# Optimization experiments

Hardware: AMD Instinct MI355X
Metric: run time of the kernel (lower is better)

Reference implementation:

```python
import jax, jax.numpy as jnp
import numpy as np

B, C, D_IN, T = 8, 4, 256, 1024
D_MODEL = 256


def setup_inputs() -> dict:
    key = jax.random.key(0)
    k_x, k_m, k_wq, k_bq, k_wo, k_bo = jax.random.split(key, 6)
    x = jax.random.normal(k_x, (B, C, D_IN, T), dtype=jnp.float32)
    mask = jax.random.randint(k_m, (B, C, T, T), 0, 2) == 1  # bool, True = masked
    s_in = 1.0 / np.sqrt(D_IN)
    s_md = 1.0 / np.sqrt(D_MODEL)
    w_qkv = jax.random.uniform(k_wq, (3 * D_MODEL, D_IN), jnp.float32, -s_in, s_in)
    b_qkv = jax.random.uniform(k_bq, (3 * D_MODEL,), jnp.float32, -s_in, s_in)
    w_out = jax.random.uniform(k_wo, (D_MODEL, D_MODEL), jnp.float32, -s_md, s_md)
    b_out = jax.random.uniform(k_bo, (D_MODEL,), jnp.float32, -s_md, s_md)
    return {"x": x, "mask": mask, "w_qkv": w_qkv, "b_qkv": b_qkv,
            "w_out": w_out, "b_out": b_out}


def reference(x, mask, w_qkv, b_qkv, w_out, b_out):
    # x: (B, C, d_in, t) -> (B, C, t, d_in)
    xt = jnp.swapaxes(x, -1, -2)
    qkv = jnp.einsum('bctd,ed->bcte', xt, w_qkv) + b_qkv  # (B,C,t,3*d_model)
    q, k, v = jnp.split(qkv, 3, axis=-1)
    scale = 1.0 / jnp.sqrt(jnp.asarray(q.shape[-1], dtype=q.dtype))
    scores = jnp.einsum('bcqd,bckd->bcqk', q, k) * scale  # (B,C,t,t)
    scores = jnp.where(mask, -jnp.inf, scores)
    attn = jax.nn.softmax(scores, axis=-1)
    out = jnp.einsum('bcqk,bckd->bcqd', attn, v)          # (B,C,t,d_model)
    return jnp.einsum('bcqd,ed->bcqe', out, w_out) + b_out
```

## Files before the change

kernel.cpp:

```cpp
#include <hip/hip_runtime.h>
#include <hip/hip_bf16.h>

#define TT 1024
#define DM 256
#define BCN 32

typedef __attribute__((ext_vector_type(8))) short short8;
typedef __attribute__((ext_vector_type(4))) short short4v;
typedef __attribute__((ext_vector_type(4))) float f32x4;

__device__ __forceinline__ void wg_barrier_lds() {
  asm volatile("s_waitcnt lgkmcnt(0)\n\ts_barrier" ::: "memory");
}

__device__ __forceinline__ short bf16b(float f) {
  __hip_bfloat16 h = __float2bfloat16(f);
  return *(short*)&h;
}

__device__ __forceinline__ void dma16(void* l, const void* g) {
  __builtin_amdgcn_global_load_lds(
      (const __attribute__((address_space(1))) void*)g,
      (__attribute__((address_space(3))) void*)l, 16, 0, 0);
}
__device__ __forceinline__ void dma4(void* l, const void* g) {
  __builtin_amdgcn_global_load_lds(
      (const __attribute__((address_space(1))) void*)g,
      (__attribute__((address_space(3))) void*)l, 4, 0, 0);
}

__global__ __launch_bounds__(256, 8) void maskprep_kernel(
    const int* __restrict__ mask, unsigned* __restrict__ mbits,
    const float* __restrict__ w_qkv, const float* __restrict__ w_out,
    __hip_bfloat16* __restrict__ Wb, __hip_bfloat16* __restrict__ Wo)
{
  const int tid = threadIdx.x;

  if (blockIdx.x >= 512) {
    int idx = (blockIdx.x - 512) * 256 + tid;
    const float* src;
    __hip_bfloat16* dst;
    if (idx < 24576) { src = w_qkv; dst = Wb; }
    else { idx -= 24576; src = w_out; dst = Wo; }
    const int r = idx >> 5, ch = idx & 31;
    const float4* wv4 = (const float4*)src + (size_t)r * 64 + ch * 2;
    const float4 f0 = wv4[0], f1 = wv4[1];
    short8 pk;
    pk[0] = bf16b(f0.x); pk[1] = bf16b(f0.y);
    pk[2] = bf16b(f0.z); pk[3] = bf16b(f0.w);
    pk[4] = bf16b(f1.x); pk[5] = bf16b(f1.y);
    pk[6] = bf16b(f1.z); pk[7] = bf16b(f1.w);
    *(short8*)&dst[(size_t)r * 256 + ((ch ^ (r & 7)) << 3)] = pk;
    return;
  }

  __shared__ unsigned Wlds[64][33];
  const int m = blockIdx.x;
  const int bc = m >> 4, q0 = (m & 15) * 64;
  const int w = tid >> 6, l = tid & 63;
  const int4* base =
      (const int4*)(mask + (size_t)(bc * 1024 + q0 + w * 16) * 1024) + l;
  int4 v[4], n[4];
#pragma unroll
  for (int s = 0; s < 4; ++s) v[s] = base[s * 64];
#pragma unroll 1
  for (int rr = 0; rr < 16; ++rr) {
    if (rr < 15) {
      const int4* nb = base + (rr + 1) * 256;
#pragma unroll
      for (int s = 0; s < 4; ++s) n[s] = nb[s * 64];
    }
    const int ql = w * 16 + rr;
#pragma unroll
    for (int s = 0; s < 4; ++s) {
      const unsigned long long bx = __ballot(v[s].x != 0);
      const unsigned long long by = __ballot(v[s].y != 0);
      const unsigned long long bz = __ballot(v[s].z != 0);
      const unsigned long long bw = __ballot(v[s].w != 0);
      if (l < 8) {
        const unsigned word =
            (unsigned)((bx >> (8 * l)) & 0xFF) |
            ((unsigned)((by >> (8 * l)) & 0xFF) << 8) |
            ((unsigned)((bz >> (8 * l)) & 0xFF) << 16) |
            ((unsigned)((bw >> (8 * l)) & 0xFF) << 24);
        Wlds[ql][s * 8 + l] = word;
      }
    }
#pragma unroll
    for (int s = 0; s < 4; ++s) v[s] = n[s];
  }
  __syncthreads();
  unsigned* mb = mbits + (size_t)bc * 32 * 1024 + q0;
#pragma unroll
  for (int i = 0; i < 8; ++i) {
    const int idx = tid + i * 256, j = idx >> 6, ql = idx & 63;
    mb[(size_t)j * 1024 + ql] = Wlds[ql][j];
  }
}

__global__ __launch_bounds__(256, 2) void qkv_kernel(
    const float* __restrict__ x, const __hip_bfloat16* __restrict__ Wb,
    const float* __restrict__ b_qkv,
    __hip_bfloat16* __restrict__ Qb, __hip_bfloat16* __restrict__ Kb,
    __hip_bfloat16* __restrict__ Vtb)
{
  const int tid = threadIdx.x;
  __shared__ __attribute__((aligned(16))) __hip_bfloat16 Xs[64][264];
  __shared__ __attribute__((aligned(16))) __hip_bfloat16 Wd[2][32 * 256];
  __shared__ __attribute__((aligned(16))) float bls[768];

  const int tt = blockIdx.x & 15, bc = blockIdx.x >> 4;
  const int t0 = tt * 64;
  const int w = tid >> 6, l = tid & 63, quad = l >> 4, lm = l & 15;
  const int lm7 = lm & 7;

  const char* Wg = (const char*)Wb;
  auto wissue = [&](int it, int buf) {
    const char* g = Wg + (size_t)it * 16384 + w * 4096 + l * 16;
    char* d = (char*)&Wd[buf][0] + w * 4096;
#pragma unroll
    for (int i = 0; i < 4; ++i) dma16(d + i * 1024, g + i * 1024);
  };

  wissue(0, 0);
  wissue(1, 1);

  if (tid < 192) {
    const float4 bv = *(const float4*)(b_qkv + tid * 4);
    *(float4*)&bls[tid * 4] = bv;
  }

  {
    const float* xbc = x + (size_t)bc * DM * TT;
    const int t4 = (tid & 15) * 4;
    for (int s = 0; s < 4; ++s) {
      const int d4 = (tid >> 4) * 4 + s * 64;
      f32x4 f[4];
#pragma unroll
      for (int r = 0; r < 4; ++r)
        f[r] = *(const f32x4*)(xbc + (size_t)(d4 + r) * TT + t0 + t4);
#pragma unroll
      for (int r = 0; r < 4; ++r) {
        short4v pk;
#pragma unroll
        for (int c = 0; c < 4; ++c) pk[c] = bf16b(f[c][r]);
        *(short4v*)&Xs[t4 + r][d4] = pk;
      }
    }
  }

#pragma unroll 1
  for (int it = 0; it < 24; ++it) {
    const int buf = it & 1;
    if (it == 0)
      asm volatile("s_waitcnt vmcnt(4)" ::: "memory");
    else if (it < 23)
      asm volatile("s_waitcnt vmcnt(6)" ::: "memory");
    else
      asm volatile("s_waitcnt vmcnt(2)" ::: "memory");
    wg_barrier_lds();

    const int e0 = it * 32;
    const bool vmode = (it >= 16);
    const __hip_bfloat16* WT = &Wd[buf][0];
    f32x4 acc[2] = {};
#pragma unroll
    for (int ks = 0; ks < 8; ++ks) {
      const int k = ks * 32 + quad * 8;
      const short8 xa = *(const short8*)&Xs[w * 16 + lm][k];
      const int c = ((ks * 4 + quad) ^ lm7) << 3;
#pragma unroll
      for (int nt = 0; nt < 2; ++nt) {
        const short8 wb2 = *(const short8*)&WT[(nt * 16 + lm) * 256 + c];
        acc[nt] = vmode
            ? __builtin_amdgcn_mfma_f32_16x16x32_bf16(xa, wb2, acc[nt], 0, 0, 0)
            : __builtin_amdgcn_mfma_f32_16x16x32_bf16(wb2, xa, acc[nt], 0, 0, 0);
      }
    }

    if (it < 8) {
      const int t = t0 + w * 16 + lm;
#pragma unroll
      for (int nt = 0; nt < 2; ++nt) {
        const int ebase = e0 + nt * 16 + quad * 4;
        const f32x4 bb = *(const f32x4*)&bls[ebase];
        short4v pk;
#pragma unroll
        for (int r = 0; r < 4; ++r) pk[r] = bf16b(acc[nt][r] + bb[r]);
        *(short4v*)&Qb[((size_t)bc * TT + t) * DM + ebase] = pk;
      }
    } else if (!vmode) {
      const int t = t0 + w * 16 + lm;
#pragma unroll
      for (int nt = 0; nt < 2; ++nt) {
        const int eg = e0 + nt * 16 + quad * 4;
        const int eK = eg - 256;
        const f32x4 bb = *(const f32x4*)&bls[eg];
        short4v pk;
#pragma unroll
        for (int r = 0; r < 4; ++r) pk[r] = bf16b(acc[nt][r] + bb[r]);
        const int ch = eK >> 3;
        const int off = (((ch ^ (t & 7)) << 3) | (eK & 7));
        *(short4v*)&Kb[((size_t)bc * TT + t) * DM + off] = pk;
      }
    } else {
      const int tb = w * 16 + quad * 4;
      const int kb = tt * 2 + (tb >> 5), tloc = tb & 31;
#pragma unroll
      for (int nt = 0; nt < 2; ++nt) {
        const int e = (e0 - 512) + nt * 16 + lm;
        const float bq = bls[512 + e];
        short4v pk;
#pragma unroll
        for (int r = 0; r < 4; ++r) pk[r] = bf16b(acc[nt][r] + bq);
        *(short4v*)&Vtb[(((size_t)bc * 32 + kb) * 256 + e) * 32 + tloc] = pk;
      }
    }

    wg_barrier_lds();
    if (it < 22) wissue(it + 2, buf);
  }
}

__global__ __launch_bounds__(256, 2) void attn_kernel(
    const __hip_bfloat16* __restrict__ Qb, const __hip_bfloat16* __restrict__ Kb,
    const __hip_bfloat16* __restrict__ Vtb, const unsigned* __restrict__ Mbits,
    const __hip_bfloat16* __restrict__ Wob, const float* __restrict__ b_out,
    float* __restrict__ out)
{
  const int fid = blockIdx.x;
  const int xcd = fid & 7, slot = fid >> 3;
  const int bc = xcd * 4 + (slot >> 4);
  const int qt = slot & 15;
  const int q0 = qt * 64;

  __shared__ __attribute__((aligned(16))) char smem[72192];
  __hip_bfloat16* Ks = (__hip_bfloat16*)smem;
  __hip_bfloat16* Vs = (__hip_bfloat16*)(smem + 32768);
  __hip_bfloat16 (*Ps)[40] = (__hip_bfloat16(*)[40])(smem + 65536);
  unsigned* Msb = (unsigned*)(smem + 70656);
  float* bout = (float*)(smem + 71168);
  __hip_bfloat16 (*Os)[264] = (__hip_bfloat16(*)[264])smem;
  __hip_bfloat16* Wo = (__hip_bfloat16*)(smem + 33792);

  const int tid = threadIdx.x, w = tid >> 6, l = tid & 63;
  const int quad = l >> 4, lm = l & 15, lm7 = lm & 7;
  const int trow = w * 16 + lm;

  if (tid < 64) {
    const f32x4 bv = *(const f32x4*)(b_out + tid * 4);
    *(f32x4*)&bout[tid * 4] = bv;
  }

  const __hip_bfloat16* Qg =
      Qb + ((size_t)bc * TT + q0 + trow) * DM + quad * 8;
  short8 qf[8];
#pragma unroll
  for (int ks = 0; ks < 8; ++ks) qf[ks] = *(const short8*)(Qg + ks * 32);

  const char* KgT = (const char*)(Kb + (size_t)bc * TT * DM);
  const char* VgT = (const char*)(Vtb + (size_t)bc * TT * DM);
  const unsigned* MgT = Mbits + ((size_t)bc * 32) * 1024 + q0;

  short8 ones;
#pragma unroll
  for (int i = 0; i < 8; ++i) ones[i] = (short)0x3F80;

  f32x4 Oa[16] = {};
  f32x4 Ol = {};

  auto issue = [&](int j, int buf) {
    const char* kg = KgT + (size_t)j * 16384 + w * 4096 + l * 16;
    const char* vg = VgT + (size_t)j * 16384 + w * 4096 + l * 16;
    char* kl = (char*)Ks + buf * 16384 + w * 4096;
    char* vl = (char*)Vs + buf * 16384 + w * 4096;
#pragma unroll
    for (int i = 0; i < 4; ++i) dma16(kl + i * 1024, kg + i * 1024);
#pragma unroll
    for (int i = 0; i < 4; ++i) dma16(vl + i * 1024, vg + i * 1024);
    dma4((char*)Msb + buf * 256, MgT + (size_t)j * 1024 + l);
  };

  auto compute = [&](int buf) {
    const __hip_bfloat16* KT = Ks + buf * 8192;
    const __hip_bfloat16* VT = Vs + buf * 8192;
    f32x4 Sa0 = {}, Sa1 = {};
#pragma unroll
    for (int ks = 0; ks < 8; ++ks) {
      const int c = ((ks * 4 + quad) ^ lm7) << 3;
      const short8 a0 = *(const short8*)&KT[lm * 256 + c];
      const short8 a1 = *(const short8*)&KT[(lm + 16) * 256 + c];
      Sa0 = __builtin_amdgcn_mfma_f32_16x16x32_bf16(a0, qf[ks], Sa0, 0, 0, 0);
      Sa1 = __builtin_amdgcn_mfma_f32_16x16x32_bf16(a1, qf[ks], Sa1, 0, 0, 0);
    }
    const unsigned mw = Msb[buf * 64 + trow];
#pragma unroll
    for (int nt = 0; nt < 2; ++nt) {
      const f32x4 Sa = nt ? Sa1 : Sa0;
      short4v pk;
#pragma unroll
      for (int r = 0; r < 4; ++r) {
        const float p = ((mw >> (nt * 4 + quad + 8 * r)) & 1u)
                            ? 0.f
                            : __expf(fmaf(Sa[r], 0.0625f, -8.0f));
        pk[r] = bf16b(p);
      }
      *(short4v*)&Ps[trow][nt * 16 + quad * 4] = pk;
    }
    const short8 pf = *(const short8*)&Ps[trow][quad * 8];
#pragma unroll
    for (int ct = 0; ct < 16; ++ct) {
      const short8 a = *(const short8*)&VT[(ct * 16 + lm) * 32 + quad * 8];
      Oa[ct] = __builtin_amdgcn_mfma_f32_16x16x32_bf16(a, pf, Oa[ct], 0, 0, 0);
    }
    Ol = __builtin_amdgcn_mfma_f32_16x16x32_bf16(ones, pf, Ol, 0, 0, 0);
  };

  issue(0, 0);
  issue(1, 1);
#pragma unroll 1
  for (int j = 0; j < 32; ++j) {
    const int buf = j & 1;
    if (j < 31)
      asm volatile("s_waitcnt vmcnt(9)" ::: "memory");
    else
      asm volatile("s_waitcnt vmcnt(0)" ::: "memory");
    asm volatile("s_barrier" ::: "memory");
    compute(buf);
    wg_barrier_lds();
    if (j < 30) issue(j + 2, buf);
  }

  const char* WoG = (const char*)Wob;
  auto pissue = [&](int it, int buf) {
    const char* g = WoG + (size_t)it * 16384 + w * 4096 + l * 16;
    char* d = (char*)Wo + buf * 16384 + w * 4096;
#pragma unroll
    for (int i = 0; i < 4; ++i) dma16(d + i * 1024, g + i * 1024);
  };
  pissue(0, 0);
  pissue(1, 1);

  const float inv = 1.0f / Ol[0];
#pragma unroll
  for (int ct = 0; ct < 16; ++ct) {
    short4v pk;
#pragma unroll
    for (int r = 0; r < 4; ++r) pk[r] = bf16b(Oa[ct][r] * inv);
    *(short4v*)&Os[trow][ct * 16 + quad * 4] = pk;
  }
  wg_barrier_lds();

  short8 osr[8];
#pragma unroll
  for (int ks = 0; ks < 8; ++ks)
    osr[ks] = *(const short8*)&Os[trow][ks * 32 + quad * 8];

  float* outp = out + ((size_t)bc * TT + q0 + trow) * DM;
#pragma unroll 1
  for (int it = 0; it < 8; ++it) {
    const int buf = it & 1;
    if (it == 0)
      asm volatile("s_waitcnt vmcnt(4)" ::: "memory");
    else if (it < 7)
      asm volatile("s_waitcnt vmcnt(6)" ::: "memory");
    else
      asm volatile("s_waitcnt vmcnt(2)" ::: "memory");
    wg_barrier_lds();

    f32x4 acc[2] = {};
#pragma unroll
    for (int ks = 0; ks < 8; ++ks) {
      const int c = ((ks * 4 + quad) ^ lm7) << 3;
#pragma unroll
      for (int nt = 0; nt < 2; ++nt) {
        const short8 wa = *(const short8*)&Wo[buf * 8192 + (nt * 16 + lm) * 256 + c];
        acc[nt] = __builtin_amdgcn_mfma_f32_16x16x32_bf16(wa, osr[ks], acc[nt], 0, 0, 0);
      }
    }
#pragma unroll
    for (int nt = 0; nt < 2; ++nt) {
      const int fb = it * 32 + nt * 16 + quad * 4;
      const f32x4 bb = *(const f32x4*)&bout[fb];
      float4 o;
      o.x = acc[nt][0] + bb[0];
      o.y = acc[nt][1] + bb[1];
      o.z = acc[nt][2] + bb[2];
      o.w = acc[nt][3] + bb[3];
      *(float4*)&outp[fb] = o;
    }

    wg_barrier_lds();
    if (it < 6) pissue(it + 2, buf);
  }
}

extern "C" void kernel_launch(void* const* d_in, const int* in_sizes, int n_in,
                              void* d_out, int out_size, void* d_ws, size_t ws_size,
                              hipStream_t stream) {
  const float* x = (const float*)d_in[0];
  const int* mask = (const int*)d_in[1];
  const float* w_qkv = (const float*)d_in[2];
  const float* b_qkv = (const float*)d_in[3];
  const float* w_out = (const float*)d_in[4];
  const float* b_out = (const float*)d_in[5];
  float* out = (float*)d_out;

  const size_t N = (size_t)BCN * TT * DM;
  __hip_bfloat16* Qb  = (__hip_bfloat16*)d_ws;
  __hip_bfloat16* Kb  = Qb + N;
  __hip_bfloat16* Vtb = Kb + N;
  unsigned* Mbits     = (unsigned*)(Vtb + N);
  __hip_bfloat16* Wbp = (__hip_bfloat16*)(Mbits + (size_t)BCN * 32 * 1024);
  __hip_bfloat16* Wob = Wbp + 768 * 256;

  maskprep_kernel<<<dim3(640), dim3(256), 0, stream>>>(mask, Mbits,
                                                       w_qkv, w_out, Wbp, Wob);
  qkv_kernel<<<dim3(512), dim3(256), 0, stream>>>(x, Wbp, b_qkv, Qb, Kb, Vtb);
  attn_kernel<<<dim3(512), dim3(256), 0, stream>>>(Qb, Kb, Vtb, Mbits,
                                                   Wob, b_out, out);
}
```

Measured before the change: 322.4 us.

## Process 128 query rows per attention block to reuse K/V tiles

Each attention workgroup now handles two 64-row query halves, sharing each loaded K/V tile and mask chunk between them and halving the grid to 256 blocks. This is meant to halve global/LDS traffic for K and V per query row. It doubles accumulator and Q-fragment registers, risking spills or lower occupancy, and leaves only one block per CU. The output projection is run twice sequentially, once per half.

```diff
diff --git a/kernel.cpp b/kernel.cpp
--- a/kernel.cpp
+++ b/kernel.cpp
@@ -230,16 +230,16 @@
 {
   const int fid = blockIdx.x;
   const int xcd = fid & 7, slot = fid >> 3;
-  const int bc = xcd * 4 + (slot >> 4);
-  const int qt = slot & 15;
-  const int q0 = qt * 64;
-
-  __shared__ __attribute__((aligned(16))) char smem[72192];
+  const int bc = xcd * 4 + (slot >> 3);
+  const int qt = slot & 7;
+  const int q0 = qt * 128;
+
+  __shared__ __attribute__((aligned(16))) char smem[77824];
   __hip_bfloat16* Ks = (__hip_bfloat16*)smem;
   __hip_bfloat16* Vs = (__hip_bfloat16*)(smem + 32768);
   __hip_bfloat16 (*Ps)[40] = (__hip_bfloat16(*)[40])(smem + 65536);
-  unsigned* Msb = (unsigned*)(smem + 70656);
-  float* bout = (float*)(smem + 71168);
+  unsigned* Msb = (unsigned*)(smem + 75776);
+  float* bout = (float*)(smem + 76800);
   __hip_bfloat16 (*Os)[264] = (__hip_bfloat16(*)[264])smem;
   __hip_bfloat16* Wo = (__hip_bfloat16*)(smem + 33792);
 
@@ -252,11 +252,14 @@
     *(f32x4*)&bout[tid * 4] = bv;
   }
 
-  const __hip_bfloat16* Qg =
-      Qb + ((size_t)bc * TT + q0 + trow) * DM + quad * 8;
-  short8 qf[8];
-#pragma unroll
-  for (int ks = 0; ks < 8; ++ks) qf[ks] = *(const short8*)(Qg + ks * 32);
+  short8 qf[2][8];
+#pragma unroll
+  for (int h = 0; h < 2; ++h) {
+    const __hip_bfloat16* Qg =
+        Qb + ((size_t)bc * TT + q0 + h * 64 + trow) * DM + quad * 8;
+#pragma unroll
+    for (int ks = 0; ks < 8; ++ks) qf[h][ks] = *(const short8*)(Qg + ks * 32);
+  }
 
   const char* KgT = (const char*)(Kb + (size_t)bc * TT * DM);
   const char* VgT = (const char*)(Vtb + (size_t)bc * TT * DM);
@@ -266,8 +269,8 @@
 #pragma unroll
   for (int i = 0; i < 8; ++i) ones[i] = (short)0x3F80;
 
-  f32x4 Oa[16] = {};
-  f32x4 Ol = {};
+  f32x4 Oa[32] = {};
+  f32x4 Ol[2] = {};
 
   auto issue = [&](int j, int buf) {
     const char* kg = KgT + (size_t)j * 16384 + w * 4096 + l * 16;
@@ -278,42 +281,51 @@
     for (int i = 0; i < 4; ++i) dma16(kl + i * 1024, kg + i * 1024);
 #pragma unroll
     for (int i = 0; i < 4; ++i) dma16(vl + i * 1024, vg + i * 1024);
-    dma4((char*)Msb + buf * 256, MgT + (size_t)j * 1024 + l);
+    dma4((char*)Msb + buf * 512, MgT + (size_t)j * 1024 + l);
+    dma4((char*)Msb + buf * 512 + 256, MgT + (size_t)j * 1024 + 64 + l);
   };
 
   auto compute = [&](int buf) {
     const __hip_bfloat16* KT = Ks + buf * 8192;
     const __hip_bfloat16* VT = Vs + buf * 8192;
-    f32x4 Sa0 = {}, Sa1 = {};
+    f32x4 Sa[2][2] = {};
 #pragma unroll
     for (int ks = 0; ks < 8; ++ks) {
       const int c = ((ks * 4 + quad) ^ lm7) << 3;
       const short8 a0 = *(const short8*)&KT[lm * 256 + c];
       const short8 a1 = *(const short8*)&KT[(lm + 16) * 256 + c];
-      Sa0 = __builtin_amdgcn_mfma_f32_16x16x32_bf16(a0, qf[ks], Sa0, 0, 0, 0);
-      Sa1 = __builtin_amdgcn_mfma_f32_16x16x32_bf16(a1, qf[ks], Sa1, 0, 0, 0);
-    }
-    const unsigned mw = Msb[buf * 64 + trow];
-#pragma unroll
-    for (int nt = 0; nt < 2; ++nt) {
-      const f32x4 Sa = nt ? Sa1 : Sa0;
-      short4v pk;
-#pragma unroll
-      for (int r = 0; r < 4; ++r) {
-        const float p = ((mw >> (nt * 4 + quad + 8 * r)) & 1u)
-                            ? 0.f
-                            : __expf(fmaf(Sa[r], 0.0625f, -8.0f));
-        pk[r] = bf16b(p);
-      }
-      *(short4v*)&Ps[trow][nt * 16 + quad * 4] = pk;
-    }
-    const short8 pf = *(const short8*)&Ps[trow][quad * 8];
-#pragma unroll
-    for (int ct = 0; ct < 16; ++ct) {
-      const short8 a = *(const short8*)&VT[(ct * 16 + lm) * 32 + quad * 8];
-      Oa[ct] = __builtin_amdgcn_mfma_f32_16x16x32_bf16(a, pf, Oa[ct], 0, 0, 0);
-    }
-    Ol = __builtin_amdgcn_mfma_f32_16x16x32_bf16(ones, pf, Ol, 0, 0, 0);
+      Sa[0][0] = __builtin_amdgcn_mfma_f32_16x16x32_bf16(a0, qf[0][ks], Sa[0][0], 0, 0, 0);
+      Sa[1][0] = __builtin_amdgcn_mfma_f32_16x16x32_bf16(a1, qf[0][ks], Sa[1][0], 0, 0, 0);
+      Sa[0][1] = __builtin_amdgcn_mfma_f32_16x16x32_bf16(a0, qf[1][ks], Sa[0][1], 0, 0, 0);
+      Sa[1][1] = __builtin_amdgcn_mfma_f32_16x16x32_bf16(a1, qf[1][ks], Sa[1][1], 0, 0, 0);
+    }
+#pragma unroll
+    for (int h = 0; h < 2; ++h) {
+      const unsigned mw = Msb[buf * 128 + h * 64 + trow];
+#pragma unroll
+      for (int nt = 0; nt < 2; ++nt) {
+        short4v pk;
+#pragma unroll
+        for (int r = 0; r < 4; ++r) {
+          const float p = ((mw >> (nt * 4 + quad + 8 * r)) & 1u)
+                              ? 0.f
+                              : __expf(fmaf(Sa[nt][h][r], 0.0625f, -8.0f));
+          pk[r] = bf16b(p);
+        }
+        *(short4v*)&Ps[h * 64 + trow][nt * 16 + quad * 4] = pk;
+      }
+    }
+#pragma unroll
+    for (int h = 0; h < 2; ++h) {
+      const short8 pf = *(const short8*)&Ps[h * 64 + trow][quad * 8];
+#pragma unroll
+      for (int ct = 0; ct < 16; ++ct) {
+        const short8 a = *(const short8*)&VT[(ct * 16 + lm) * 32 + quad * 8];
+        Oa[h * 16 + ct] =
+            __builtin_amdgcn_mfma_f32_16x16x32_bf16(a, pf, Oa[h * 16 + ct], 0, 0, 0);
+      }
+      Ol[h] = __builtin_amdgcn_mfma_f32_16x16x32_bf16(ones, pf, Ol[h], 0, 0, 0);
+    }
   };
 
   issue(0, 0);
@@ -322,7 +334,7 @@
   for (int j = 0; j < 32; ++j) {
     const int buf = j & 1;
     if (j < 31)
-      asm volatile("s_waitcnt vmcnt(9)" ::: "memory");
+      asm volatile("s_waitcnt vmcnt(10)" ::: "memory");
     else
       asm volatile("s_waitcnt vmcnt(0)" ::: "memory");
     asm volatile("s_barrier" ::: "memory");
@@ -338,60 +350,66 @@
 #pragma unroll
     for (int i = 0; i < 4; ++i) dma16(d + i * 1024, g + i * 1024);
   };
-  pissue(0, 0);
-  pissue(1, 1);
-
-  const float inv = 1.0f / Ol[0];
-#pragma unroll
-  for (int ct = 0; ct < 16; ++ct) {
-    short4v pk;
-#pragma unroll
-    for (int r = 0; r < 4; ++r) pk[r] = bf16b(Oa[ct][r] * inv);
-    *(short4v*)&Os[trow][ct * 16 + quad * 4] = pk;
-  }
-  wg_barrier_lds();
-
-  short8 osr[8];
-#pragma unroll
-  for (int ks = 0; ks < 8; ++ks)
-    osr[ks] = *(const short8*)&Os[trow][ks * 32 + quad * 8];
-
-  float* outp = out + ((size_t)bc * TT + q0 + trow) * DM;
+
+#pragma unroll
+  for (int h = 0; h < 2; ++h) {
+    pissue(0, 0);
+    pissue(1, 1);
+
+    const float inv = 1.0f / Ol[h][0];
+#pragma unroll
+    for (int ct = 0; ct < 16; ++ct) {
+      short4v pk;
+#pragma unroll
+      for (int r = 0; r < 4; ++r) pk[r] = bf16b(Oa[h * 16 + ct][r] * inv);
+      *(short4v*)&Os[trow][ct * 16 + quad * 4] = pk;
+    }
+    wg_barrier_lds();
+
+    short8 osr[8];
+#pragma unroll
+    for (int ks = 0; ks < 8; ++ks)
+      osr[ks] = *(const short8*)&Os[trow][ks * 32 + quad * 8];
+
+    float* outp = out + ((size_t)bc * TT + q0 + h * 64 + trow) * DM;
 #pragma unroll 1
-  for (int it = 0; it < 8; ++it) {
-    const int buf = it & 1;
-    if (it == 0)
-      asm volatile("s_waitcnt vmcnt(4)" ::: "memory");
-    else if (it < 7)
-      asm volatile("s_waitcnt vmcnt(6)" ::: "memory");
-    else
-      asm volatile("s_waitcnt vmcnt(2)" ::: "memory");
-    wg_barrier_lds();
-
-    f32x4 acc[2] = {};
-#pragma unroll
-    for (int ks = 0; ks < 8; ++ks) {
-      const int c = ((ks * 4 + quad) ^ lm7) << 3;
-#pragma unroll
-      for (int nt = 0; nt < 2; ++nt) {
-        const short8 wa = *(const short8*)&Wo[buf * 8192 + (nt * 16 + lm) * 256 + c];
-        acc[nt] = __builtin_amdgcn_mfma_f32_16x16x32_bf16(wa, osr[ks], acc[nt], 0, 0, 0);
-      }
-    }
-#pragma unroll
-    for (int nt = 0; nt < 2; ++nt) {
-      const int fb = it * 32 + nt * 16 + quad * 4;
-      const f32x4 bb = *(const f32x4*)&bout[fb];
-      float4 o;
-      o.x = acc[nt][0] + bb[0];
-      o.y = acc[nt][1] + bb[1];
-      o.z = acc[nt][2] + bb[2];
-      o.w = acc[nt][3] + bb[3];
-      *(float4*)&outp[fb] = o;
-    }
-
-    wg_barrier_lds();
-    if (it < 6) pissue(it + 2, buf);
+    for (int it = 0; it < 8; ++it) {
+      const int buf = it & 1;
+      if (it == 0)
+        asm volatile("s_waitcnt vmcnt(4)" ::: "memory");
+      else if (it < 7)
+        asm volatile("s_waitcnt vmcnt(6)" ::: "memory");
+      else
+        asm volatile("s_waitcnt vmcnt(2)" ::: "memory");
+      wg_barrier_lds();
+
+      f32x4 acc[2] = {};
+#pragma unroll
+      for (int ks = 0; ks < 8; ++ks) {
+        const int c = ((ks * 4 + quad) ^ lm7) << 3;
+#pragma unroll
+        for (int nt = 0; nt < 2; ++nt) {
+          const short8 wa =
+              *(const short8*)&Wo[buf * 8192 + (nt * 16 + lm) * 256 + c];
+          acc[nt] =
+              __builtin_amdgcn_mfma_f32_16x16x32_bf16(wa, osr[ks], acc[nt], 0, 0, 0);
+        }
+      }
+#pragma unroll
+      for (int nt = 0; nt < 2; ++nt) {
+        const int fb = it * 32 + nt * 16 + quad * 4;
+        const f32x4 bb = *(const f32x4*)&bout[fb];
+        float4 o;
+        o.x = acc[nt][0] + bb[0];
+        o.y = acc[nt][1] + bb[1];
+        o.z = acc[nt][2] + bb[2];
+        o.w = acc[nt][3] + bb[3];
+        *(float4*)&outp[fb] = o;
+      }
+
+      wg_barrier_lds();
+      if (it < 6) pissue(it + 2, buf);
+    }
   }
 }
 
@@ -417,6 +435,6 @@
   maskprep_kernel<<<dim3(640), dim3(256), 0, stream>>>(mask, Mbits,
                                                        w_qkv, w_out, Wbp, Wob);
   qkv_kernel<<<dim3(512), dim3(256), 0, stream>>>(x, Wbp, b_qkv, Qb, Kb, Vtb);
-  attn_kernel<<<dim3(512), dim3(256), 0, stream>>>(Qb, Kb, Vtb, Mbits,
+  attn_kernel<<<dim3(256), dim3(256), 0, stream>>>(Qb, Kb, Vtb, Mbits,
                                                    Wob, b_out, out);
 }
```

Result: slower. 380.2 us (+17.9%).
